# Kernel tuning notes

Measured on AMD Instinct MI355X. Metric: run time of the kernel, lower is better.

Reference implementation:

```python
import jax, jax.numpy as jnp
import numpy as np


def setup_inputs() -> dict:
    key = jax.random.key(0)
    k1, k2 = jax.random.split(key)
    B, L, D = 8, 2048, 128
    query = jax.random.normal(k1, (B, L, D), dtype=jnp.float32)
    value = jax.random.normal(k2, (B, L, D), dtype=jnp.float32)
    return {"query": query, "value": value}


def reference(query, value):
    # scores: [B, Lq, Lk] = query @ value^T (note: NO 1/sqrt(d) scaling, key == value)
    scores = jnp.einsum("bqd,bkd->bqk", query, value)
    weights = jax.nn.softmax(scores, axis=-1)
    # context: [B, Lq, D]
    context = jnp.einsum("bqk,bkd->bqd", weights, value)
    return context
```

## Files before the change

kernel.cpp:

```cpp
#include <hip/hip_runtime.h>
#include <hip/hip_fp16.h>

typedef _Float16 f16;
typedef __attribute__((ext_vector_type(8))) _Float16 f16x8;
typedef __attribute__((ext_vector_type(4))) _Float16 f16x4;
typedef __attribute__((ext_vector_type(4))) short s16x4;
typedef __attribute__((ext_vector_type(4))) float f32x4;
typedef __attribute__((ext_vector_type(2))) float f32x2;

#define MFMA16(a,b,c) __builtin_amdgcn_mfma_f32_16x16x32_f16(a,b,c,0,0,0)
#define EXP2(x) __builtin_amdgcn_exp2f(x)
#define LOG2E 1.4426950408889634f

#define B_DIM 8
#define L_DIM 2048
#define D_DIM 128
#define NGRP 4
#define KVB 64
#define NTILES 8
#define TILE_B 16384
#define P_ST 72
#define SLAB_ST 132
#define SMEM_B 137216

__device__ __forceinline__ unsigned ldsa(const void* p) {
    return (unsigned)(unsigned long long)(const __attribute__((address_space(3))) char*)p;
}

#define TRRD(d, a, O) asm volatile("ds_read_b64_tr_b16 %0, %1 offset:" O : "=v"(d) : "v"(a))
#define LGKM0() do { asm volatile("s_waitcnt lgkmcnt(0)" ::: "memory"); __builtin_amdgcn_sched_barrier(0); } while (0)
#define GLDS(gp, lp) __builtin_amdgcn_global_load_lds( \
    (const __attribute__((address_space(1))) unsigned int*)(gp), \
    (__attribute__((address_space(3))) unsigned int*)(lp), 16, 0, 0)

#define PVND(TL, TH, PA0, PA1, ND) { \
    union { s16x4 s2[2]; f16x8 v; } uu; uu.s2[0] = TL; uu.s2[1] = TH; \
    acc[0][ND] = MFMA16(PA0, uu.v, acc[0][ND]); \
    acc[1][ND] = MFMA16(PA1, uu.v, acc[1][ND]); }

#define PV_HALF(AREG, PA0, PA1, S0,S0b,S1,S1b,S2,S2b,S3,S3b, NDB) { \
    s16x4 t0l,t0h,t1l,t1h,t2l,t2h,t3l,t3h; \
    TRRD(t0l, AREG, S0);  TRRD(t0h, AREG, S0b); \
    TRRD(t1l, AREG, S1);  TRRD(t1h, AREG, S1b); \
    TRRD(t2l, AREG, S2);  TRRD(t2h, AREG, S2b); \
    TRRD(t3l, AREG, S3);  TRRD(t3h, AREG, S3b); \
    LGKM0(); \
    __builtin_amdgcn_s_setprio(1); \
    PVND(t0l, t0h, PA0, PA1, NDB+0); PVND(t1l, t1h, PA0, PA1, NDB+1); \
    PVND(t2l, t2h, PA0, PA1, NDB+2); PVND(t3l, t3h, PA0, PA1, NDB+3); \
    __builtin_amdgcn_s_setprio(0); }

__global__ __launch_bounds__(256) void prep_v(const float* __restrict__ V, f16* __restrict__ ws) {
    const int blk = blockIdx.x;
    const float* src = V + (size_t)blk * (KVB * D_DIM);
    f16* dst = ws + (size_t)blk * (KVB * D_DIM);
    const int t = threadIdx.x;
    #pragma unroll
    for (int ii = 0; ii < 4; ++ii) {
        int lin = ii * 256 + t;
        int kv = lin >> 4, oct = lin & 15;
        const float* sp = src + kv * D_DIM + oct * 8;
        f32x4 a = *(const f32x4*)sp;
        f32x4 b = *(const f32x4*)(sp + 4);
        int c = (kv >> 2) * 64 + (oct >> 1) * 8 + (kv & 3) * 2 + (oct & 1);
        union { f16 h[8]; f16x8 v; } u;
        #pragma unroll
        for (int k = 0; k < 4; ++k) { u.h[k] = (f16)a[k]; u.h[k + 4] = (f16)b[k]; }
        *(f16x8*)(dst + (size_t)c * 8) = u.v;
    }
}

__global__ __launch_bounds__(512, 2) void attn_fwd(
    const float* __restrict__ Q, const f16* __restrict__ ws, float* __restrict__ Out)
{
    __shared__ __align__(16) char smem[SMEM_B];

    const int tid  = threadIdx.x;
    const int wv   = tid >> 6;
    const int grp  = wv >> 1;
    const int qw   = wv & 1;
    const int lane = tid & 63;
    const int lrow = lane & 15;
    const int g    = lane >> 4;

    const int blk = blockIdx.x;
    const int b   = blk & 7;
    const int q0  = (blk >> 3) * 64;

    char* grpbase = smem + grp * (2 * TILE_B);

    f16x8 qh[2][4];
    {
        const float* qb = Q + ((size_t)b * L_DIM + q0 + qw * 32) * D_DIM;
        #pragma unroll
        for (int q2 = 0; q2 < 2; ++q2) {
            const float* qp = qb + (size_t)(q2 * 16 + lrow) * D_DIM + g * 8;
            #pragma unroll
            for (int dt = 0; dt < 4; ++dt) {
                f32x4 f0 = *(const f32x4*)(qp + dt * 32);
                f32x4 f1 = *(const f32x4*)(qp + dt * 32 + 4);
                #pragma unroll
                for (int i = 0; i < 4; ++i) {
                    qh[q2][dt][i]     = (f16)(f0[i] * LOG2E);
                    qh[q2][dt][i + 4] = (f16)(f1[i] * LOG2E);
                }
            }
        }
    }

    f32x4 acc[2][8];
    #pragma unroll
    for (int q2 = 0; q2 < 2; ++q2)
        #pragma unroll
        for (int i = 0; i < 8; ++i) acc[q2][i] = (f32x4)0.0f;
    float m_run[2] = { -3.0e38f, -3.0e38f }, l_run[2] = { 0.0f, 0.0f };

    const int qkoff = (lrow >> 2) * 1024 + (g >> 1) * 128 + (lrow & 3) * 32 + (g & 1) * 16;

    const f16* wsb = ws + (size_t)b * (32 * KVB * D_DIM);

    {
        const f16* w0 = wsb + (size_t)(grp * 8) * 8192 + (size_t)(qw * 512 + lane) * 8;
        char* ldst = grpbase + qw * 8192;
        #pragma unroll
        for (int i = 0; i < 8; ++i) GLDS(w0 + i * 512, ldst + i * 1024);
    }
    __syncthreads();

    for (int t = 0; t < NTILES; ++t) {
        const int c = t & 1;
        char* cur = grpbase + c * TILE_B;
        char* alt = grpbase + (c ^ 1) * TILE_B;

        f32x4 s[2][4];
        #pragma unroll
        for (int q2 = 0; q2 < 2; ++q2)
            #pragma unroll
            for (int nt = 0; nt < 4; ++nt) s[q2][nt] = (f32x4)0.0f;
        __builtin_amdgcn_s_setprio(1);
        #pragma unroll
        for (int nt = 0; nt < 4; ++nt) {
            #pragma unroll
            for (int dt = 0; dt < 4; ++dt) {
                f16x8 a = *(const f16x8*)(cur + qkoff + nt * 4096 + dt * 256);
                s[0][nt] = MFMA16(a, qh[0][dt], s[0][nt]);
                s[1][nt] = MFMA16(a, qh[1][dt], s[1][nt]);
            }
        }
        __builtin_amdgcn_s_setprio(0);

        float pm[2];
        #pragma unroll
        for (int q2 = 0; q2 < 2; ++q2) {
            float tm = s[q2][0][0];
            #pragma unroll
            for (int nt = 0; nt < 4; ++nt)
                #pragma unroll
                for (int r = 0; r < 4; ++r) tm = fmaxf(tm, s[q2][nt][r]);
            tm = fmaxf(tm, __shfl_xor(tm, 16));
            tm = fmaxf(tm, __shfl_xor(tm, 32));
            pm[q2] = tm;
        }
        bool need = (pm[0] > m_run[0] + 11.5f) || (pm[1] > m_run[1] + 11.5f);
        if (__any(need)) {
            float scl[2];
            #pragma unroll
            for (int q2 = 0; q2 < 2; ++q2) {
                float mnew = fmaxf(m_run[q2], pm[q2]);
                scl[q2]  = EXP2(m_run[q2] - mnew);
                m_run[q2] = mnew;
                l_run[q2] *= scl[q2];
            }
            float sr[2][4];
            #pragma unroll
            for (int r = 0; r < 4; ++r) {
                sr[0][r] = __shfl(scl[0], g * 4 + r);
                sr[1][r] = __shfl(scl[1], g * 4 + r);
            }
            #pragma unroll
            for (int q2 = 0; q2 < 2; ++q2)
                #pragma unroll
                for (int nd = 0; nd < 8; ++nd)
                    #pragma unroll
                    for (int r = 0; r < 4; ++r) acc[q2][nd][r] *= sr[q2][r];
        }
        #pragma unroll
        for (int q2 = 0; q2 < 2; ++q2) {
            float ps = 0.0f;
            #pragma unroll
            for (int nt = 0; nt < 4; ++nt)
                #pragma unroll
                for (int r = 0; r < 4; ++r) {
                    float p = EXP2(s[q2][nt][r] - m_run[q2]);
                    s[q2][nt][r] = p;
                    ps += p;
                }
            ps += __shfl_xor(ps, 16);
            ps += __shfl_xor(ps, 32);
            l_run[q2] += ps;
        }

        f16* pls = (f16*)(alt + qw * 8192);
        #pragma unroll
        for (int q2 = 0; q2 < 2; ++q2) {
            #pragma unroll
            for (int nt = 0; nt < 4; ++nt) {
                f16x4 w = { (f16)s[q2][nt][0], (f16)s[q2][nt][1],
                            (f16)s[q2][nt][2], (f16)s[q2][nt][3] };
                *(f16x4*)(pls + (size_t)(q2 * 16 + lrow) * P_ST + nt * 16 + g * 4) = w;
            }
        }
        f16x8 pa00, pa01, pa10, pa11;
        pa00 = *(const f16x8*)(pls + (size_t)(lrow) * P_ST + g * 8);
        pa01 = *(const f16x8*)(pls + (size_t)(lrow) * P_ST + 32 + g * 8);
        pa10 = *(const f16x8*)(pls + (size_t)(16 + lrow) * P_ST + g * 8);
        pa11 = *(const f16x8*)(pls + (size_t)(16 + lrow) * P_ST + 32 + g * 8);
        LGKM0();

        if (t + 1 < NTILES) {
            const f16* wnt = wsb + (size_t)(grp * 8 + t + 1) * 8192 + (size_t)(qw * 512 + lane) * 8;
            char* ldst = alt + qw * 8192;
            #pragma unroll
            for (int i = 0; i < 8; ++i) GLDS(wnt + i * 512, ldst + i * 1024);
        }

        unsigned atr0 = ldsa(cur) + (unsigned)(g * 2048 + lrow * 8);
        unsigned atr1 = atr0 + 8192u;
        PV_HALF(atr0, pa00, pa10, "0","1024","128","1152","256","1280","384","1408", 0);
        PV_HALF(atr0, pa00, pa10, "512","1536","640","1664","768","1792","896","1920", 4);
        PV_HALF(atr1, pa01, pa11, "0","1024","128","1152","256","1280","384","1408", 0);
        PV_HALF(atr1, pa01, pa11, "512","1536","640","1664","768","1792","896","1920", 4);

        __syncthreads();
    }

    float* slab = (float*)smem;
    float* mlp  = (float*)(smem + 8 * 32 * SLAB_ST * 4);
    #pragma unroll
    for (int q2 = 0; q2 < 2; ++q2)
        #pragma unroll
        for (int nd = 0; nd < 8; ++nd)
            #pragma unroll
            for (int r = 0; r < 4; ++r)
                slab[(size_t)(wv * 32 + q2 * 16 + g * 4 + r) * SLAB_ST + nd * 16 + lrow] = acc[q2][nd][r];
    if (g == 0) {
        #pragma unroll
        for (int q2 = 0; q2 < 2; ++q2) {
            mlp[wv * 64 + q2 * 16 + lrow]      = m_run[q2];
            mlp[wv * 64 + 32 + q2 * 16 + lrow] = l_run[q2];
        }
    }
    __syncthreads();

    #pragma unroll
    for (int rr = 0; rr < 8; ++rr) {
        int row = wv * 8 + rr;
        int qws = row >> 5, ql = row & 31;
        float mg[4], M = -3.0e38f;
        #pragma unroll
        for (int gg = 0; gg < 4; ++gg) {
            mg[gg] = mlp[(gg * 2 + qws) * 64 + ql];
            M = fmaxf(M, mg[gg]);
        }
        float L = 0.0f, f[4];
        #pragma unroll
        for (int gg = 0; gg < 4; ++gg) {
            f[gg] = EXP2(mg[gg] - M);
            L += f[gg] * mlp[(gg * 2 + qws) * 64 + 32 + ql];
        }
        float inv = 1.0f / L;
        f32x2 o = { 0.0f, 0.0f };
        #pragma unroll
        for (int gg = 0; gg < 4; ++gg) {
            f32x2 v = *(const f32x2*)&slab[(size_t)((gg * 2 + qws) * 32 + ql) * SLAB_ST + lane * 2];
            o[0] += f[gg] * v[0];
            o[1] += f[gg] * v[1];
        }
        o[0] *= inv; o[1] *= inv;
        *(f32x2*)&Out[((size_t)b * L_DIM + q0 + row) * D_DIM + lane * 2] = o;
    }
}

extern "C" void kernel_launch(void* const* d_in, const int* in_sizes, int n_in,
                              void* d_out, int out_size, void* d_ws, size_t ws_size,
                              hipStream_t stream) {
    const float* Q = (const float*)d_in[0];
    const float* V = (const float*)d_in[1];
    float* Out     = (float*)d_out;
    f16* ws        = (f16*)d_ws;
    prep_v<<<dim3(B_DIM * (L_DIM / KVB)), dim3(256), 0, stream>>>(V, ws);
    attn_fwd<<<dim3(B_DIM * (L_DIM / 64)), dim3(512), 0, stream>>>(Q, ws, Out);
}
```

Before: 39.13 us.

## Halve query and KV tile sizes to double grid size and occupancy

Each block now handles 32 query rows instead of 64 (16 per wave), and KV tiles shrink from 64 to 32 keys with 16 tiles per group. LDS use drops to about 67 KB so four blocks of 512 threads can share a CU, and the grid doubles to 512 blocks to fill the device better. The epilogue is rewritten so each thread reduces and writes 8 contiguous output floats. In exchange, each query block re-reads V twice as often from L2, and there are more loop iterations and barriers per unit of MFMA work.

Measured after the change: 45.76 us. +16.9%, slower.

```diff
diff --git a/kernel.cpp b/kernel.cpp
--- a/kernel.cpp
+++ b/kernel.cpp
@@ -16,12 +16,14 @@
 #define L_DIM 2048
 #define D_DIM 128
 #define NGRP 4
-#define KVB 64
-#define NTILES 8
-#define TILE_B 16384
-#define P_ST 72
-#define SLAB_ST 132
-#define SMEM_B 137216
+#define KVB 32
+#define NTILES 16
+#define TILE_B 8192
+#define TILE_H 4096
+#define P_ST 40
+#define SLAB_ST 129
+#define SLAB_B (8 * 16 * SLAB_ST * 4)
+#define SMEM_B (SLAB_B + 1024)
 
 __device__ __forceinline__ unsigned ldsa(const void* p) {
     return (unsigned)(unsigned long long)(const __attribute__((address_space(3))) char*)p;
@@ -33,12 +35,11 @@
     (const __attribute__((address_space(1))) unsigned int*)(gp), \
     (__attribute__((address_space(3))) unsigned int*)(lp), 16, 0, 0)
 
-#define PVND(TL, TH, PA0, PA1, ND) { \
+#define PVND(TL, TH, PA, ND) { \
     union { s16x4 s2[2]; f16x8 v; } uu; uu.s2[0] = TL; uu.s2[1] = TH; \
-    acc[0][ND] = MFMA16(PA0, uu.v, acc[0][ND]); \
-    acc[1][ND] = MFMA16(PA1, uu.v, acc[1][ND]); }
-
-#define PV_HALF(AREG, PA0, PA1, S0,S0b,S1,S1b,S2,S2b,S3,S3b, NDB) { \
+    acc[ND] = MFMA16(PA, uu.v, acc[ND]); }
+
+#define PV_HALF(AREG, PA, S0,S0b,S1,S1b,S2,S2b,S3,S3b, NDB) { \
     s16x4 t0l,t0h,t1l,t1h,t2l,t2h,t3l,t3h; \
     TRRD(t0l, AREG, S0);  TRRD(t0h, AREG, S0b); \
     TRRD(t1l, AREG, S1);  TRRD(t1h, AREG, S1b); \
@@ -46,17 +47,17 @@
     TRRD(t3l, AREG, S3);  TRRD(t3h, AREG, S3b); \
     LGKM0(); \
     __builtin_amdgcn_s_setprio(1); \
-    PVND(t0l, t0h, PA0, PA1, NDB+0); PVND(t1l, t1h, PA0, PA1, NDB+1); \
-    PVND(t2l, t2h, PA0, PA1, NDB+2); PVND(t3l, t3h, PA0, PA1, NDB+3); \
+    PVND(t0l, t0h, PA, NDB+0); PVND(t1l, t1h, PA, NDB+1); \
+    PVND(t2l, t2h, PA, NDB+2); PVND(t3l, t3h, PA, NDB+3); \
     __builtin_amdgcn_s_setprio(0); }
 
 __global__ __launch_bounds__(256) void prep_v(const float* __restrict__ V, f16* __restrict__ ws) {
     const int blk = blockIdx.x;
     const float* src = V + (size_t)blk * (KVB * D_DIM);
-    f16* dst = ws + (size_t)blk * (KVB * D_DIM);
+    f16* dst = ws + (size_t)blk * TILE_H;
     const int t = threadIdx.x;
     #pragma unroll
-    for (int ii = 0; ii < 4; ++ii) {
+    for (int ii = 0; ii < 2; ++ii) {
         int lin = ii * 256 + t;
         int kv = lin >> 4, oct = lin & 15;
         const float* sp = src + kv * D_DIM + oct * 8;
@@ -70,7 +71,7 @@
     }
 }
 
-__global__ __launch_bounds__(512, 2) void attn_fwd(
+__global__ __launch_bounds__(512, 4) void attn_fwd(
     const float* __restrict__ Q, const f16* __restrict__ ws, float* __restrict__ Out)
 {
     __shared__ __align__(16) char smem[SMEM_B];
@@ -85,45 +86,39 @@
 
     const int blk = blockIdx.x;
     const int b   = blk & 7;
-    const int q0  = (blk >> 3) * 64;
+    const int q0  = (blk >> 3) * 32;
 
     char* grpbase = smem + grp * (2 * TILE_B);
 
-    f16x8 qh[2][4];
+    f16x8 qh[4];
     {
-        const float* qb = Q + ((size_t)b * L_DIM + q0 + qw * 32) * D_DIM;
-        #pragma unroll
-        for (int q2 = 0; q2 < 2; ++q2) {
-            const float* qp = qb + (size_t)(q2 * 16 + lrow) * D_DIM + g * 8;
-            #pragma unroll
-            for (int dt = 0; dt < 4; ++dt) {
-                f32x4 f0 = *(const f32x4*)(qp + dt * 32);
-                f32x4 f1 = *(const f32x4*)(qp + dt * 32 + 4);
-                #pragma unroll
-                for (int i = 0; i < 4; ++i) {
-                    qh[q2][dt][i]     = (f16)(f0[i] * LOG2E);
-                    qh[q2][dt][i + 4] = (f16)(f1[i] * LOG2E);
-                }
+        const float* qp = Q + ((size_t)b * L_DIM + q0 + qw * 16 + lrow) * D_DIM + g * 8;
+        #pragma unroll
+        for (int dt = 0; dt < 4; ++dt) {
+            f32x4 f0 = *(const f32x4*)(qp + dt * 32);
+            f32x4 f1 = *(const f32x4*)(qp + dt * 32 + 4);
+            #pragma unroll
+            for (int i = 0; i < 4; ++i) {
+                qh[dt][i]     = (f16)(f0[i] * LOG2E);
+                qh[dt][i + 4] = (f16)(f1[i] * LOG2E);
             }
         }
     }
 
-    f32x4 acc[2][8];
+    f32x4 acc[8];
     #pragma unroll
-    for (int q2 = 0; q2 < 2; ++q2)
-        #pragma unroll
-        for (int i = 0; i < 8; ++i) acc[q2][i] = (f32x4)0.0f;
-    float m_run[2] = { -3.0e38f, -3.0e38f }, l_run[2] = { 0.0f, 0.0f };
+    for (int i = 0; i < 8; ++i) acc[i] = (f32x4)0.0f;
+    float m_run = -3.0e38f, l_run = 0.0f;
 
     const int qkoff = (lrow >> 2) * 1024 + (g >> 1) * 128 + (lrow & 3) * 32 + (g & 1) * 16;
 
-    const f16* wsb = ws + (size_t)b * (32 * KVB * D_DIM);
+    const f16* wst = ws + (size_t)b * (64 * TILE_H) + (size_t)(grp * NTILES) * TILE_H;
 
     {
-        const f16* w0 = wsb + (size_t)(grp * 8) * 8192 + (size_t)(qw * 512 + lane) * 8;
-        char* ldst = grpbase + qw * 8192;
-        #pragma unroll
-        for (int i = 0; i < 8; ++i) GLDS(w0 + i * 512, ldst + i * 1024);
+        const f16* w0 = wst + qw * 2048 + lane * 8;
+        char* l0 = grpbase + qw * 4096;
+        #pragma unroll
+        for (int i = 0; i < 4; ++i) GLDS(w0 + i * 512, l0 + i * 1024);
     }
     __syncthreads();
 
@@ -132,152 +127,122 @@
         char* cur = grpbase + c * TILE_B;
         char* alt = grpbase + (c ^ 1) * TILE_B;
 
-        f32x4 s[2][4];
-        #pragma unroll
-        for (int q2 = 0; q2 < 2; ++q2)
-            #pragma unroll
-            for (int nt = 0; nt < 4; ++nt) s[q2][nt] = (f32x4)0.0f;
+        f32x4 s[2];
+        s[0] = (f32x4)0.0f; s[1] = (f32x4)0.0f;
         __builtin_amdgcn_s_setprio(1);
         #pragma unroll
-        for (int nt = 0; nt < 4; ++nt) {
+        for (int nt = 0; nt < 2; ++nt) {
             #pragma unroll
             for (int dt = 0; dt < 4; ++dt) {
                 f16x8 a = *(const f16x8*)(cur + qkoff + nt * 4096 + dt * 256);
-                s[0][nt] = MFMA16(a, qh[0][dt], s[0][nt]);
-                s[1][nt] = MFMA16(a, qh[1][dt], s[1][nt]);
+                s[nt] = MFMA16(a, qh[dt], s[nt]);
             }
         }
         __builtin_amdgcn_s_setprio(0);
 
-        float pm[2];
-        #pragma unroll
-        for (int q2 = 0; q2 < 2; ++q2) {
-            float tm = s[q2][0][0];
-            #pragma unroll
-            for (int nt = 0; nt < 4; ++nt)
+        float tm = s[0][0];
+        #pragma unroll
+        for (int nt = 0; nt < 2; ++nt)
+            #pragma unroll
+            for (int r = 0; r < 4; ++r) tm = fmaxf(tm, s[nt][r]);
+        tm = fmaxf(tm, __shfl_xor(tm, 16));
+        tm = fmaxf(tm, __shfl_xor(tm, 32));
+        bool need = (tm > m_run + 11.5f);
+        if (__any(need)) {
+            float mnew = fmaxf(m_run, tm);
+            float scl  = EXP2(m_run - mnew);
+            m_run = mnew;
+            l_run *= scl;
+            float sr[4];
+            #pragma unroll
+            for (int r = 0; r < 4; ++r) sr[r] = __shfl(scl, g * 4 + r);
+            #pragma unroll
+            for (int nd = 0; nd < 8; ++nd)
                 #pragma unroll
-                for (int r = 0; r < 4; ++r) tm = fmaxf(tm, s[q2][nt][r]);
-            tm = fmaxf(tm, __shfl_xor(tm, 16));
-            tm = fmaxf(tm, __shfl_xor(tm, 32));
-            pm[q2] = tm;
-        }
-        bool need = (pm[0] > m_run[0] + 11.5f) || (pm[1] > m_run[1] + 11.5f);
-        if (__any(need)) {
-            float scl[2];
-            #pragma unroll
-            for (int q2 = 0; q2 < 2; ++q2) {
-                float mnew = fmaxf(m_run[q2], pm[q2]);
-                scl[q2]  = EXP2(m_run[q2] - mnew);
-                m_run[q2] = mnew;
-                l_run[q2] *= scl[q2];
-            }
-            float sr[2][4];
-            #pragma unroll
-            for (int r = 0; r < 4; ++r) {
-                sr[0][r] = __shfl(scl[0], g * 4 + r);
-                sr[1][r] = __shfl(scl[1], g * 4 + r);
-            }
-            #pragma unroll
-            for (int q2 = 0; q2 < 2; ++q2)
-                #pragma unroll
-                for (int nd = 0; nd < 8; ++nd)
-                    #pragma unroll
-                    for (int r = 0; r < 4; ++r) acc[q2][nd][r] *= sr[q2][r];
-        }
-        #pragma unroll
-        for (int q2 = 0; q2 < 2; ++q2) {
+                for (int r = 0; r < 4; ++r) acc[nd][r] *= sr[r];
+        }
+        {
             float ps = 0.0f;
             #pragma unroll
-            for (int nt = 0; nt < 4; ++nt)
+            for (int nt = 0; nt < 2; ++nt)
                 #pragma unroll
                 for (int r = 0; r < 4; ++r) {
-                    float p = EXP2(s[q2][nt][r] - m_run[q2]);
-                    s[q2][nt][r] = p;
+                    float p = EXP2(s[nt][r] - m_run);
+                    s[nt][r] = p;
                     ps += p;
                 }
             ps += __shfl_xor(ps, 16);
             ps += __shfl_xor(ps, 32);
-            l_run[q2] += ps;
-        }
-
-        f16* pls = (f16*)(alt + qw * 8192);
-        #pragma unroll
-        for (int q2 = 0; q2 < 2; ++q2) {
-            #pragma unroll
-            for (int nt = 0; nt < 4; ++nt) {
-                f16x4 w = { (f16)s[q2][nt][0], (f16)s[q2][nt][1],
-                            (f16)s[q2][nt][2], (f16)s[q2][nt][3] };
-                *(f16x4*)(pls + (size_t)(q2 * 16 + lrow) * P_ST + nt * 16 + g * 4) = w;
-            }
-        }
-        f16x8 pa00, pa01, pa10, pa11;
-        pa00 = *(const f16x8*)(pls + (size_t)(lrow) * P_ST + g * 8);
-        pa01 = *(const f16x8*)(pls + (size_t)(lrow) * P_ST + 32 + g * 8);
-        pa10 = *(const f16x8*)(pls + (size_t)(16 + lrow) * P_ST + g * 8);
-        pa11 = *(const f16x8*)(pls + (size_t)(16 + lrow) * P_ST + 32 + g * 8);
+            l_run += ps;
+        }
+
+        f16* pls = (f16*)(alt + qw * 4096);
+        #pragma unroll
+        for (int nt = 0; nt < 2; ++nt) {
+            f16x4 w = { (f16)s[nt][0], (f16)s[nt][1], (f16)s[nt][2], (f16)s[nt][3] };
+            *(f16x4*)(pls + (size_t)lrow * P_ST + nt * 16 + g * 4) = w;
+        }
+        f16x8 pa = *(const f16x8*)(pls + (size_t)lrow * P_ST + g * 8);
         LGKM0();
 
         if (t + 1 < NTILES) {
-            const f16* wnt = wsb + (size_t)(grp * 8 + t + 1) * 8192 + (size_t)(qw * 512 + lane) * 8;
-            char* ldst = alt + qw * 8192;
-            #pragma unroll
-            for (int i = 0; i < 8; ++i) GLDS(wnt + i * 512, ldst + i * 1024);
+            const f16* wnt = wst + (size_t)(t + 1) * TILE_H + qw * 2048 + lane * 8;
+            char* ldst = alt + qw * 4096;
+            #pragma unroll
+            for (int i = 0; i < 4; ++i) GLDS(wnt + i * 512, ldst + i * 1024);
         }
 
         unsigned atr0 = ldsa(cur) + (unsigned)(g * 2048 + lrow * 8);
-        unsigned atr1 = atr0 + 8192u;
-        PV_HALF(atr0, pa00, pa10, "0","1024","128","1152","256","1280","384","1408", 0);
-        PV_HALF(atr0, pa00, pa10, "512","1536","640","1664","768","1792","896","1920", 4);
-        PV_HALF(atr1, pa01, pa11, "0","1024","128","1152","256","1280","384","1408", 0);
-        PV_HALF(atr1, pa01, pa11, "512","1536","640","1664","768","1792","896","1920", 4);
+        PV_HALF(atr0, pa, "0","1024","128","1152","256","1280","384","1408", 0);
+        PV_HALF(atr0, pa, "512","1536","640","1664","768","1792","896","1920", 4);
 
         __syncthreads();
     }
 
     float* slab = (float*)smem;
-    float* mlp  = (float*)(smem + 8 * 32 * SLAB_ST * 4);
+    float* mlp  = (float*)(smem + SLAB_B);
     #pragma unroll
-    for (int q2 = 0; q2 < 2; ++q2)
-        #pragma unroll
-        for (int nd = 0; nd < 8; ++nd)
-            #pragma unroll
-            for (int r = 0; r < 4; ++r)
-                slab[(size_t)(wv * 32 + q2 * 16 + g * 4 + r) * SLAB_ST + nd * 16 + lrow] = acc[q2][nd][r];
+    for (int nd = 0; nd < 8; ++nd)
+        #pragma unroll
+        for (int r = 0; r < 4; ++r)
+            slab[(size_t)(wv * 16 + g * 4 + r) * SLAB_ST + nd * 16 + lrow] = acc[nd][r];
     if (g == 0) {
-        #pragma unroll
-        for (int q2 = 0; q2 < 2; ++q2) {
-            mlp[wv * 64 + q2 * 16 + lrow]      = m_run[q2];
-            mlp[wv * 64 + 32 + q2 * 16 + lrow] = l_run[q2];
-        }
+        mlp[wv * 32 + lrow]      = m_run;
+        mlp[wv * 32 + 16 + lrow] = l_run;
     }
     __syncthreads();
 
-    #pragma unroll
-    for (int rr = 0; rr < 8; ++rr) {
-        int row = wv * 8 + rr;
-        int qws = row >> 5, ql = row & 31;
+    {
+        int row = tid >> 4;
+        int dc  = (tid & 15) * 8;
+        int qwo = row >> 4, rr = row & 15;
         float mg[4], M = -3.0e38f;
         #pragma unroll
         for (int gg = 0; gg < 4; ++gg) {
-            mg[gg] = mlp[(gg * 2 + qws) * 64 + ql];
+            mg[gg] = mlp[(gg * 2 + qwo) * 32 + rr];
             M = fmaxf(M, mg[gg]);
         }
         float L = 0.0f, f[4];
         #pragma unroll
         for (int gg = 0; gg < 4; ++gg) {
             f[gg] = EXP2(mg[gg] - M);
-            L += f[gg] * mlp[(gg * 2 + qws) * 64 + 32 + ql];
+            L += f[gg] * mlp[(gg * 2 + qwo) * 32 + 16 + rr];
         }
         float inv = 1.0f / L;
-        f32x2 o = { 0.0f, 0.0f };
+        float o[8];
+        #pragma unroll
+        for (int j = 0; j < 8; ++j) o[j] = 0.0f;
         #pragma unroll
         for (int gg = 0; gg < 4; ++gg) {
-            f32x2 v = *(const f32x2*)&slab[(size_t)((gg * 2 + qws) * 32 + ql) * SLAB_ST + lane * 2];
-            o[0] += f[gg] * v[0];
-            o[1] += f[gg] * v[1];
-        }
-        o[0] *= inv; o[1] *= inv;
-        *(f32x2*)&Out[((size_t)b * L_DIM + q0 + row) * D_DIM + lane * 2] = o;
+            const float* sp = &slab[(size_t)((gg * 2 + qwo) * 16 + rr) * SLAB_ST + dc];
+            #pragma unroll
+            for (int j = 0; j < 8; ++j) o[j] += f[gg] * sp[j];
+        }
+        f32x4 o0 = { o[0] * inv, o[1] * inv, o[2] * inv, o[3] * inv };
+        f32x4 o1 = { o[4] * inv, o[5] * inv, o[6] * inv, o[7] * inv };
+        float* op = Out + ((size_t)b * L_DIM + q0 + row) * D_DIM + dc;
+        *(f32x4*)op = o0;
+        *(f32x4*)(op + 4) = o1;
     }
 }
 
@@ -289,5 +254,5 @@
     float* Out     = (float*)d_out;
     f16* ws        = (f16*)d_ws;
     prep_v<<<dim3(B_DIM * (L_DIM / KVB)), dim3(256), 0, stream>>>(V, ws);
-    attn_fwd<<<dim3(B_DIM * (L_DIM / 64)), dim3(512), 0, stream>>>(Q, ws, Out);
-}
+    attn_fwd<<<dim3(B_DIM * (L_DIM / 32)), dim3(512), 0, stream>>>(Q, ws, Out);
+}
```
